# Kernel tuning notes

Measured on AMD Instinct MI355X. Metric: run time of the kernel, lower is better.

The kernel has to match this reference:

```python
import jax, jax.numpy as jnp
import numpy as np

N_NODES = 50000
N_EDGES = 800000
N_GRAPHS = 2000
N_PAIRS = 4096
IN_CH = 64
EMB = 128
HID = 256
OUT = 1


def gcn_conv(x, edge_index, W, b):
    # PyG GCNConv: h = x @ W^T, then D^{-1/2}(A+I)D^{-1/2} h + b
    h = x @ W.T                                  # [N, out]
    row, col = edge_index[0], edge_index[1]
    ones = jnp.ones((edge_index.shape[1],), h.dtype)
    deg = jax.ops.segment_sum(ones, col, num_segments=N_NODES) + 1.0  # self-loop
    dinv = jax.lax.rsqrt(deg)
    norm = dinv[row] * dinv[col]                 # [E]
    agg = jax.ops.segment_sum(h[row] * norm[:, None], col, num_segments=N_NODES)
    agg = agg + h * (1.0 / deg)[:, None]         # self-loop term (dinv[i]^2)
    return agg + b


def setup_inputs() -> dict:
    key = jax.random.key(0)
    ks = jax.random.split(key, 10)
    x = jax.random.normal(ks[0], (N_NODES, IN_CH), jnp.float32)
    edge_index = jax.random.randint(ks[1], (2, N_EDGES), 0, N_NODES, jnp.int64)
    batch = jnp.sort(jax.random.randint(ks[2], (N_NODES,), 0, N_GRAPHS, jnp.int64))
    drug_drug_batch = jax.random.randint(ks[3], (2, N_PAIRS), 0, N_GRAPHS, jnp.int64)

    def xavier(k, shape):
        fan_out, fan_in = shape
        lim = jnp.sqrt(6.0 / (fan_in + fan_out))
        return jax.random.uniform(k, shape, jnp.float32, -lim, lim)

    return {
        "x": x, "edge_index": edge_index, "batch": batch,
        "drug_drug_batch": drug_drug_batch,
        "conv1_w": xavier(ks[4], (EMB, IN_CH)), "conv1_b": jnp.zeros((EMB,), jnp.float32),
        "conv2_w": xavier(ks[5], (EMB, EMB)), "conv2_b": jnp.zeros((EMB,), jnp.float32),
        "reg1_w": xavier(ks[6], (HID, 2 * EMB)), "reg1_b": jnp.zeros((HID,), jnp.float32),
        "reg2_w": xavier(ks[7], (OUT, HID)), "reg2_b": jnp.zeros((OUT,), jnp.float32),
    }


def reference(x, edge_index, batch, drug_drug_batch,
              conv1_w, conv1_b, conv2_w, conv2_b,
              reg1_w, reg1_b, reg2_w, reg2_b):
    h = jax.nn.relu(gcn_conv(x, edge_index, conv1_w, conv1_b))
    h = jax.nn.relu(gcn_conv(h, edge_index, conv2_w, conv2_b))

    # scatter_mean readout over graphs
    gsum = jax.ops.segment_sum(h, batch, num_segments=N_GRAPHS)
    cnt = jax.ops.segment_sum(jnp.ones((N_NODES,), h.dtype), batch, num_segments=N_GRAPHS)
    graph_embeds = gsum / jnp.maximum(cnt, 1.0)[:, None]

    # quantize drug ids to dense graph indices (np.digitize on unique+1, as in source)
    dd = np.asarray(drug_drug_batch)
    bins = np.unique(dd.flatten()) + 1
    q = jnp.asarray(np.digitize(dd, bins))       # [2, P]

    pairs = jnp.concatenate([graph_embeds[q[0]], graph_embeds[q[1]]], axis=1)  # [P, 2*EMB]
    out = jax.nn.relu(pairs @ reg1_w.T + reg1_b)
    return out @ reg2_w.T + reg2_b
```

## Files before the change

### kernel.cpp

```cpp
#include <hip/hip_runtime.h>

#define N_NODES  50000
#define N_PAD    50048
#define N_EDGES  800000
#define N_GRAPHS 2000
#define N_PAIRS  4096
#define IN_CH    64
#define EMB      128
#define HID      256
#define PPB      16

__global__ void k_zero(float4* __restrict__ p, int n4) {
    int i = blockIdx.x * 256 + threadIdx.x;
    if (i < n4) p[i] = make_float4(0.f, 0.f, 0.f, 0.f);
}

__global__ void k_pre(const int* __restrict__ col, const int* __restrict__ batch,
                      const float* __restrict__ w1, const float* __restrict__ w2,
                      int* __restrict__ deg, int* __restrict__ pos_e, int* __restrict__ cnt,
                      float* __restrict__ wt1, float* __restrict__ wt2) {
    int e = blockIdx.x * 256 + threadIdx.x;
    if (e < N_EDGES) {
        int c = col[e];
        pos_e[e] = atomicAdd(&deg[c], 1);
    }
    if (e < N_NODES) atomicAdd(&cnt[batch[e]], 1);
    if (e < EMB * IN_CH) {
        int j = e / IN_CH, k = e % IN_CH;
        wt1[k * EMB + j] = w1[e];
    } else if (e < EMB * IN_CH + EMB * EMB) {
        int t = e - EMB * IN_CH;
        int j = t / EMB, k = t % EMB;
        wt2[k * EMB + j] = w2[t];
    }
}

__device__ inline int wave_incl_scan(int x, int lane) {
    #pragma unroll
    for (int off = 1; off < 64; off <<= 1) {
        int y = __shfl_up(x, off, 64);
        if (lane >= off) x += y;
    }
    return x;
}

__global__ void k_scan1(const int* __restrict__ in, int* __restrict__ part, int n) {
    __shared__ int ws[4];
    int i = blockIdx.x * 256 + threadIdx.x;
    int lane = threadIdx.x & 63, wid = threadIdx.x >> 6;
    int v = (i < n) ? in[i] : 0;
    int x = wave_incl_scan(v, lane);
    if (lane == 63) ws[wid] = x;
    __syncthreads();
    if (threadIdx.x == 0) part[blockIdx.x] = ws[0] + ws[1] + ws[2] + ws[3];
}

__global__ void k_scan2d(int* __restrict__ part, int nb,
                         const int* __restrict__ dd, int* __restrict__ rankx) {
    int t = threadIdx.x, lane = t & 63, wid = t >> 6;
    if (blockIdx.x == 0) {
        __shared__ int ws[4];
        int v = (t < nb) ? part[t] : 0;
        int x = wave_incl_scan(v, lane);
        if (lane == 63) ws[wid] = x;
        __syncthreads();
        int add = 0;
        for (int w = 0; w < wid; ++w) add += ws[w];
        if (t < nb) part[t] = x - v + add;
    } else {
        __shared__ int pres[N_GRAPHS];
        __shared__ int ws2[4];
        __shared__ int carry;
        for (int i = t; i < N_GRAPHS; i += 256) pres[i] = 0;
        __syncthreads();
        for (int i = t; i < 2 * N_PAIRS; i += 256) pres[dd[i]] = 1;
        if (t == 0) carry = 0;
        __syncthreads();
        for (int base = 0; base < N_GRAPHS; base += 256) {
            int i = base + t;
            int v = (i < N_GRAPHS) ? pres[i] : 0;
            int x = wave_incl_scan(v, lane);
            if (lane == 63) ws2[wid] = x;
            __syncthreads();
            int add = carry;
            for (int w = 0; w < wid; ++w) add += ws2[w];
            if (i < N_GRAPHS) rankx[i] = x - v + add;
            __syncthreads();
            if (t == 255) carry = add + x;
            __syncthreads();
        }
    }
}

__global__ void k_scan3d(const int* __restrict__ in, const int* __restrict__ part,
                         int* __restrict__ off, float* __restrict__ dinv) {
    __shared__ int ws[4];
    int i = blockIdx.x * 256 + threadIdx.x;
    int lane = threadIdx.x & 63, wid = threadIdx.x >> 6;
    int v = (i < N_NODES) ? in[i] : 0;
    int x = wave_incl_scan(v, lane);
    if (lane == 63) ws[wid] = x;
    __syncthreads();
    int add = part[blockIdx.x];
    for (int w = 0; w < wid; ++w) add += ws[w];
    if (i < N_NODES) {
        off[i] = x - v + add;
        dinv[i] = 1.0f / sqrtf((float)(v + 1));
    }
    if (i == 0) off[N_NODES] = N_EDGES;
}

__global__ void k_fill_scale(const int* __restrict__ row, const int* __restrict__ col,
                             const int* __restrict__ pos_e, const int* __restrict__ off,
                             int* __restrict__ csr_row,
                             const float4* __restrict__ x, const float* __restrict__ dinv,
                             float4* __restrict__ xs) {
    int idx = blockIdx.x * 256 + threadIdx.x;
    if (idx < N_EDGES) {
        int c = col[idx];
        int p = pos_e[idx];
        csr_row[off[c] + p] = row[idx];
    } else {
        int i = idx - N_EDGES;
        int n = i >> 4;
        float d = dinv[n];
        float4 v = x[i];
        v.x *= d; v.y *= d; v.z *= d; v.w *= d;
        xs[i] = v;
    }
}

__device__ inline void f4add(float4& a, const float4 b) {
    a.x += b.x; a.y += b.y; a.z += b.z; a.w += b.w;
}

template <int C>
__global__ void k_gather8(const float4* __restrict__ hs, const int* __restrict__ csr_row,
                          const int* __restrict__ off, const float* __restrict__ dinv,
                          float4* __restrict__ out) {
    constexpr int L = C / 4;
    constexpr int NPB = 256 / L;
    int local = threadIdx.x / L;
    int c4 = threadIdx.x % L;
    int n = blockIdx.x * NPB + local;
    int s = off[n], e = off[n + 1];
    float4 acc = hs[n * L + c4];
    int i = s;
    for (; i + 8 <= e; i += 8) {
        int r0 = csr_row[i + 0], r1 = csr_row[i + 1], r2 = csr_row[i + 2], r3 = csr_row[i + 3];
        int r4 = csr_row[i + 4], r5 = csr_row[i + 5], r6 = csr_row[i + 6], r7 = csr_row[i + 7];
        float4 a0 = hs[r0 * L + c4], a1 = hs[r1 * L + c4];
        float4 a2 = hs[r2 * L + c4], a3 = hs[r3 * L + c4];
        float4 a4 = hs[r4 * L + c4], a5 = hs[r5 * L + c4];
        float4 a6 = hs[r6 * L + c4], a7 = hs[r7 * L + c4];
        f4add(a0, a1); f4add(a2, a3); f4add(a4, a5); f4add(a6, a7);
        f4add(a0, a2); f4add(a4, a6);
        f4add(a0, a4);
        f4add(acc, a0);
    }
    for (; i < e; ++i) {
        int r = csr_row[i];
        float4 a = hs[r * L + c4];
        f4add(acc, a);
    }
    float dn = dinv[n];
    acc.x *= dn; acc.y *= dn; acc.z *= dn; acc.w *= dn;
    out[n * L + c4] = acc;
}

template <int K, bool RELU, bool BIAS, bool POSTSCALE>
__global__ void k_gemmv5(const float* __restrict__ A, const float* __restrict__ Wt,
                         const float* __restrict__ bias, const float* __restrict__ rowscale,
                         float* __restrict__ out) {
    __shared__ __align__(16) float a_lds[64 * K];
    int t = threadIdx.x;
    {
        const float4* Ag = reinterpret_cast<const float4*>(A + (size_t)blockIdx.x * 64 * K);
        float4* Al = reinterpret_cast<float4*>(a_lds);
        constexpr int NV = (64 * K) / (4 * 256);
        #pragma unroll
        for (int i = 0; i < NV; ++i) Al[t + i * 256] = Ag[t + i * 256];
    }
    __syncthreads();
    int cq = (t & 31) << 2;
    int rg = t >> 5;
    float4 acc[8];
    #pragma unroll
    for (int r = 0; r < 8; ++r) acc[r] = make_float4(0.f, 0.f, 0.f, 0.f);
    #pragma unroll 2
    for (int k = 0; k < K; k += 4) {
        float4 w0 = *reinterpret_cast<const float4*>(&Wt[(k + 0) * EMB + cq]);
        float4 w1 = *reinterpret_cast<const float4*>(&Wt[(k + 1) * EMB + cq]);
        float4 w2 = *reinterpret_cast<const float4*>(&Wt[(k + 2) * EMB + cq]);
        float4 w3 = *reinterpret_cast<const float4*>(&Wt[(k + 3) * EMB + cq]);
        #pragma unroll
        for (int r = 0; r < 8; ++r) {
            float4 a = *reinterpret_cast<const float4*>(&a_lds[(rg * 8 + r) * K + k]);
            acc[r].x = fmaf(a.x, w0.x, fmaf(a.y, w1.x, fmaf(a.z, w2.x, fmaf(a.w, w3.x, acc[r].x))));
            acc[r].y = fmaf(a.x, w0.y, fmaf(a.y, w1.y, fmaf(a.z, w2.y, fmaf(a.w, w3.y, acc[r].y))));
            acc[r].z = fmaf(a.x, w0.z, fmaf(a.y, w1.z, fmaf(a.z, w2.z, fmaf(a.w, w3.z, acc[r].z))));
            acc[r].w = fmaf(a.x, w0.w, fmaf(a.y, w1.w, fmaf(a.z, w2.w, fmaf(a.w, w3.w, acc[r].w))));
        }
    }
    int row0 = blockIdx.x * 64 + rg * 8;
    #pragma unroll
    for (int r = 0; r < 8; ++r) {
        int row = row0 + r;
        if (row < N_NODES) {
            float4 v = acc[r];
            if (BIAS) {
                float4 b = *reinterpret_cast<const float4*>(&bias[cq]);
                v.x += b.x; v.y += b.y; v.z += b.z; v.w += b.w;
            }
            if (RELU) {
                v.x = fmaxf(v.x, 0.f); v.y = fmaxf(v.y, 0.f);
                v.z = fmaxf(v.z, 0.f); v.w = fmaxf(v.w, 0.f);
            }
            if (POSTSCALE) {
                float sc = rowscale[row];
                v.x *= sc; v.y *= sc; v.z *= sc; v.w *= sc;
            }
            *reinterpret_cast<float4*>(&out[(size_t)row * EMB + cq]) = v;
        }
    }
}

template <int HALF>
__global__ void k_gro_h(const float4* __restrict__ t2, const int* __restrict__ csr_row,
                        const int* __restrict__ off, const float* __restrict__ dinv,
                        const float* __restrict__ bias, const int* __restrict__ batch,
                        float* __restrict__ gsum) {
    constexpr int NPB = 16;
    __shared__ __align__(16) float hb[NPB][64];
    __shared__ int bg[NPB];
    int t = threadIdx.x;
    int local = t >> 4;
    int c4 = t & 15;
    int n0 = blockIdx.x * NPB;
    int n = n0 + local;
    if (t < NPB) bg[t] = batch[n0 + t];
    int s = off[n], e = off[n + 1];
    const int cidx = HALF * 16 + c4;
    float4 acc = t2[(size_t)n * 32 + cidx];
    int i = s;
    for (; i + 8 <= e; i += 8) {
        int r0 = csr_row[i + 0], r1 = csr_row[i + 1], r2 = csr_row[i + 2], r3 = csr_row[i + 3];
        int r4 = csr_row[i + 4], r5 = csr_row[i + 5], r6 = csr_row[i + 6], r7 = csr_row[i + 7];
        float4 a0 = t2[(size_t)r0 * 32 + cidx], a1 = t2[(size_t)r1 * 32 + cidx];
        float4 a2 = t2[(size_t)r2 * 32 + cidx], a3 = t2[(size_t)r3 * 32 + cidx];
        float4 a4 = t2[(size_t)r4 * 32 + cidx], a5 = t2[(size_t)r5 * 32 + cidx];
        float4 a6 = t2[(size_t)r6 * 32 + cidx], a7 = t2[(size_t)r7 * 32 + cidx];
        f4add(a0, a1); f4add(a2, a3); f4add(a4, a5); f4add(a6, a7);
        f4add(a0, a2); f4add(a4, a6);
        f4add(a0, a4);
        f4add(acc, a0);
    }
    for (; i < e; ++i) {
        float4 a = t2[(size_t)csr_row[i] * 32 + cidx];
        f4add(acc, a);
    }
    float dn = dinv[n];
    float4 b = reinterpret_cast<const float4*>(bias)[cidx];
    acc.x = fmaxf(fmaf(acc.x, dn, b.x), 0.f);
    acc.y = fmaxf(fmaf(acc.y, dn, b.y), 0.f);
    acc.z = fmaxf(fmaf(acc.z, dn, b.z), 0.f);
    acc.w = fmaxf(fmaf(acc.w, dn, b.w), 0.f);
    *reinterpret_cast<float4*>(&hb[local][c4 * 4]) = acc;
    __syncthreads();
    {
        int ch = t & 63, q = t >> 6;
        int j0 = q * 4;
        int g = bg[j0];
        float a = 0.f;
        #pragma unroll
        for (int j = j0; j < j0 + 4; ++j) {
            int gj = bg[j];
            if (gj != g) { atomicAdd(&gsum[g * EMB + HALF * 64 + ch], a); a = 0.f; g = gj; }
            a += hb[j][ch];
        }
        atomicAdd(&gsum[g * EMB + HALF * 64 + ch], a);
    }
}

__global__ void k_mlp16(const float* __restrict__ gemb, const int* __restrict__ cnt,
                        const int* __restrict__ dd, const int* __restrict__ rankx,
                        const float* __restrict__ w1, const float* __restrict__ b1,
                        const float* __restrict__ w2, const float* __restrict__ b2,
                        float* __restrict__ out) {
    __shared__ __align__(16) float pv[PPB][2 * EMB];
    __shared__ float wpart[4][PPB];
    int p0 = blockIdx.x * PPB;
    int t = threadIdx.x;
    int lane = t & 63, wid = t >> 6;
    #pragma unroll
    for (int j = 0; j < PPB; ++j) {
        int p = p0 + j;
        if (t < EMB) {
            int ga = rankx[dd[p]];
            int ca = cnt[ga];
            float ra = 1.0f / (float)(ca > 1 ? ca : 1);
            pv[j][t] = gemb[ga * EMB + t] * ra;
        } else {
            int gb = rankx[dd[N_PAIRS + p]];
            int cb = cnt[gb];
            float rb = 1.0f / (float)(cb > 1 ? cb : 1);
            pv[j][t] = gemb[gb * EMB + (t - EMB)] * rb;
        }
    }
    __syncthreads();
    float acc[PPB];
    float bv = b1[t];
    #pragma unroll
    for (int j = 0; j < PPB; ++j) acc[j] = bv;
    const float4* wrow = reinterpret_cast<const float4*>(&w1[t * 2 * EMB]);
    for (int k = 0; k < (2 * EMB) / 4; ++k) {
        float4 w = wrow[k];
        #pragma unroll
        for (int j = 0; j < PPB; ++j) {
            const float4 xv = *reinterpret_cast<const float4*>(&pv[j][k * 4]);
            acc[j] = fmaf(xv.x, w.x, fmaf(xv.y, w.y, fmaf(xv.z, w.z, fmaf(xv.w, w.w, acc[j]))));
        }
    }
    float w2t = w2[t];
    float contrib[PPB];
    #pragma unroll
    for (int j = 0; j < PPB; ++j) contrib[j] = fmaxf(acc[j], 0.f) * w2t;
    #pragma unroll
    for (int off = 32; off > 0; off >>= 1) {
        #pragma unroll
        for (int j = 0; j < PPB; ++j) contrib[j] += __shfl_down(contrib[j], off, 64);
    }
    if (lane == 0) {
        #pragma unroll
        for (int j = 0; j < PPB; ++j) wpart[wid][j] = contrib[j];
    }
    __syncthreads();
    if (t < PPB) {
        out[p0 + t] = wpart[0][t] + wpart[1][t] + wpart[2][t] + wpart[3][t] + b2[0];
    }
}

extern "C" void kernel_launch(void* const* d_in, const int* in_sizes, int n_in,
                              void* d_out, int out_size, void* d_ws, size_t ws_size,
                              hipStream_t stream) {
    const float* x        = (const float*)d_in[0];
    const int*   ei       = (const int*)d_in[1];
    const int*   batch    = (const int*)d_in[2];
    const int*   dd       = (const int*)d_in[3];
    const float* conv1_w  = (const float*)d_in[4];
    const float* conv1_b  = (const float*)d_in[5];
    const float* conv2_w  = (const float*)d_in[6];
    const float* conv2_b  = (const float*)d_in[7];
    const float* reg1_w   = (const float*)d_in[8];
    const float* reg1_b   = (const float*)d_in[9];
    const float* reg2_w   = (const float*)d_in[10];
    const float* reg2_b   = (const float*)d_in[11];
    float* outp = (float*)d_out;

    const int* ei_row = ei;
    const int* ei_col = ei + N_EDGES;

    char* ws = (char*)d_ws;
    size_t o = 0;
    auto alloc = [&](size_t bytes) -> void* {
        void* p = ws + o;
        o = (o + bytes + 255) & ~(size_t)255;
        return p;
    };
    size_t zero_start = o;
    int*   deg     = (int*)alloc(N_NODES * 4);
    int*   cnt     = (int*)alloc(N_GRAPHS * 4);
    float* gsum    = (float*)alloc(N_GRAPHS * EMB * 4);
    size_t zero_bytes = o - zero_start;
    int*   off     = (int*)alloc((N_NODES + 1) * 4);
    float* dinv    = (float*)alloc(N_NODES * 4);
    int*   part    = (int*)alloc(256 * 4);
    int*   pos_e   = (int*)alloc(N_EDGES * 4);
    int*   csr_row = (int*)alloc(N_EDGES * 4);
    int*   rankx   = (int*)alloc(N_GRAPHS * 4);
    float* Wt1     = (float*)alloc(IN_CH * EMB * 4);
    float* Wt2     = (float*)alloc(EMB * EMB * 4);
    float* aggx    = (float*)alloc((size_t)N_PAD * IN_CH * 4);
    float* h1s     = (float*)alloc((size_t)N_PAD * EMB * 4);
    float* t2      = (float*)alloc((size_t)N_PAD * EMB * 4);
    float* xs      = t2;

    (void)ws_size; (void)in_sizes; (void)n_in; (void)out_size;

    {
        int n4 = (int)(zero_bytes / 16);
        k_zero<<<(n4 + 255) / 256, 256, 0, stream>>>((float4*)(ws + zero_start), n4);
    }

    k_pre<<<N_EDGES / 256, 256, 0, stream>>>(ei_col, batch, conv1_w, conv2_w,
                                             deg, pos_e, cnt, Wt1, Wt2);
    {
        int nb = (N_NODES + 255) / 256;
        k_scan1<<<nb, 256, 0, stream>>>(deg, part, N_NODES);
        k_scan2d<<<2, 256, 0, stream>>>(part, nb, dd, rankx);
        k_scan3d<<<nb, 256, 0, stream>>>(deg, part, off, dinv);
    }
    k_fill_scale<<<(N_EDGES + N_NODES * (IN_CH / 4)) / 256, 256, 0, stream>>>(
        ei_row, ei_col, pos_e, off, csr_row, (const float4*)x, dinv, (float4*)xs);

    k_gather8<IN_CH><<<N_NODES / (256 / (IN_CH / 4)), 256, 0, stream>>>(
        (const float4*)xs, csr_row, off, dinv, (float4*)aggx);
    k_gemmv5<IN_CH, true, true, true><<<N_PAD / 64, 256, 0, stream>>>(
        aggx, Wt1, conv1_b, dinv, h1s);

    k_gemmv5<EMB, false, false, false><<<N_PAD / 64, 256, 0, stream>>>(
        h1s, Wt2, nullptr, nullptr, t2);
    k_gro_h<0><<<N_NODES / 16, 256, 0, stream>>>(
        (const float4*)t2, csr_row, off, dinv, conv2_b, batch, gsum);
    k_gro_h<1><<<N_NODES / 16, 256, 0, stream>>>(
        (const float4*)t2, csr_row, off, dinv, conv2_b, batch, gsum);

    k_mlp16<<<N_PAIRS / PPB, 256, 0, stream>>>(gsum, cnt, dd, rankx,
                                               reg1_w, reg1_b, reg2_w, reg2_b, outp);
}
```

Before: 241.0 us.

## Replace global-atomic degree histogram with windowed shared-memory histograms

The old preprocessing kernel ran one thread per edge and did a global atomicAdd on the node degree to get each edge's slot. It is replaced by 25 blocks of 1024 threads. Each block owns a 2048-node window, scans the full column array, and counts edges into that window with LDS atomics, then writes the degrees out directly. Two more blocks build the per-graph counts and four blocks transpose the weights. This removes the contended global atomics and the need to zero the degree array, but every window block re-reads the whole column array, and only 31 blocks run across the device.

```diff
diff --git a/kernel.cpp b/kernel.cpp
--- a/kernel.cpp
+++ b/kernel.cpp
@@ -9,29 +9,62 @@
 #define EMB      128
 #define HID      256
 #define PPB      16
+#define WIN      2048
+#define NWIN     25
 
 __global__ void k_zero(float4* __restrict__ p, int n4) {
     int i = blockIdx.x * 256 + threadIdx.x;
     if (i < n4) p[i] = make_float4(0.f, 0.f, 0.f, 0.f);
 }
 
-__global__ void k_pre(const int* __restrict__ col, const int* __restrict__ batch,
-                      const float* __restrict__ w1, const float* __restrict__ w2,
-                      int* __restrict__ deg, int* __restrict__ pos_e, int* __restrict__ cnt,
-                      float* __restrict__ wt1, float* __restrict__ wt2) {
-    int e = blockIdx.x * 256 + threadIdx.x;
-    if (e < N_EDGES) {
-        int c = col[e];
-        pos_e[e] = atomicAdd(&deg[c], 1);
-    }
-    if (e < N_NODES) atomicAdd(&cnt[batch[e]], 1);
-    if (e < EMB * IN_CH) {
-        int j = e / IN_CH, k = e % IN_CH;
-        wt1[k * EMB + j] = w1[e];
-    } else if (e < EMB * IN_CH + EMB * EMB) {
-        int t = e - EMB * IN_CH;
-        int j = t / EMB, k = t % EMB;
-        wt2[k * EMB + j] = w2[t];
+__global__ __launch_bounds__(1024) void k_hist(
+        const int* __restrict__ col, const int* __restrict__ batch,
+        const float* __restrict__ w1, const float* __restrict__ w2,
+        int* __restrict__ deg, int* __restrict__ pos_e, int* __restrict__ cnt,
+        float* __restrict__ wt1, float* __restrict__ wt2) {
+    int b = blockIdx.x, t = threadIdx.x;
+    if (b < NWIN) {
+        __shared__ int hist[WIN];
+        int base = b * WIN;
+        for (int j = t; j < WIN; j += 1024) hist[j] = 0;
+        __syncthreads();
+        int i = t;
+        #pragma unroll 1
+        for (int k = 0; k < 195; ++k, i += 4096) {
+            int c0 = col[i + 0];
+            int c1 = col[i + 1024];
+            int c2 = col[i + 2048];
+            int c3 = col[i + 3072];
+            int l0 = c0 - base, l1 = c1 - base, l2 = c2 - base, l3 = c3 - base;
+            if ((unsigned)l0 < (unsigned)WIN) pos_e[i + 0]    = atomicAdd(&hist[l0], 1);
+            if ((unsigned)l1 < (unsigned)WIN) pos_e[i + 1024] = atomicAdd(&hist[l1], 1);
+            if ((unsigned)l2 < (unsigned)WIN) pos_e[i + 2048] = atomicAdd(&hist[l2], 1);
+            if ((unsigned)l3 < (unsigned)WIN) pos_e[i + 3072] = atomicAdd(&hist[l3], 1);
+        }
+        for (; i < N_EDGES; i += 1024) {
+            int c = col[i];
+            int l = c - base;
+            if ((unsigned)l < (unsigned)WIN) pos_e[i] = atomicAdd(&hist[l], 1);
+        }
+        __syncthreads();
+        for (int j = t; j < WIN; j += 1024) {
+            int n = base + j;
+            if (n < N_NODES) deg[n] = hist[j];
+        }
+    } else if (b < NWIN + 2) {
+        for (int i = (b - NWIN) * 1024 + t; i < N_NODES; i += 2048)
+            atomicAdd(&cnt[batch[i]], 1);
+    } else {
+        for (int i = (b - NWIN - 2) * 1024 + t; i < EMB * IN_CH + EMB * EMB; i += 4096) {
+            if (i < EMB * IN_CH) {
+                int j = i / IN_CH, k = i % IN_CH;
+                wt1[k * EMB + j] = w1[i];
+            } else {
+                int q = i - EMB * IN_CH;
+                int j = q / EMB, k = q % EMB;
+                wt2[k * EMB + j] = w2[q];
+            }
+        }
     }
 }
 
@@ -368,10 +401,10 @@
         return p;
     };
     size_t zero_start = o;
-    int*   deg     = (int*)alloc(N_NODES * 4);
     int*   cnt     = (int*)alloc(N_GRAPHS * 4);
     float* gsum    = (float*)alloc(N_GRAPHS * EMB * 4);
     size_t zero_bytes = o - zero_start;
+    int*   deg     = (int*)alloc(N_NODES * 4);
     int*   off     = (int*)alloc((N_NODES + 1) * 4);
     float* dinv    = (float*)alloc(N_NODES * 4);
     int*   part    = (int*)alloc(256 * 4);
@@ -392,8 +425,8 @@
         k_zero<<<(n4 + 255) / 256, 256, 0, stream>>>((float4*)(ws + zero_start), n4);
     }
 
-    k_pre<<<N_EDGES / 256, 256, 0, stream>>>(ei_col, batch, conv1_w, conv2_w,
-                                             deg, pos_e, cnt, Wt1, Wt2);
+    k_hist<<<NWIN + 2 + 4, 1024, 0, stream>>>(ei_col, batch, conv1_w, conv2_w,
+                                              deg, pos_e, cnt, Wt1, Wt2);
     {
         int nb = (N_NODES + 255) / 256;
         k_scan1<<<nb, 256, 0, stream>>>(deg, part, N_NODES);
```

New measurement: 404.1 us. 1.68x slower.
